# Kernel tuning notes

Measured on AMD Instinct MI355X. Metric: run time of the kernel, lower is better.

## Reference

```python
import jax, jax.numpy as jnp
import numpy as np

B, Q, K, D = 64, 2048, 2048, 128
NEG = -1e9


def setup_inputs() -> dict:
    key = jax.random.key(0)
    kq, kk, kv, kl = jax.random.split(key, 4)
    return {
        "queries": jax.random.normal(kq, (B, Q, D), dtype=jnp.float32),
        "keys": jax.random.normal(kk, (B, K, D), dtype=jnp.float32),
        "values": jax.random.normal(kv, (B, K, D), dtype=jnp.float32),
        "valid_lens": jax.random.randint(kl, (B,), 0, K, dtype=jnp.int32),
    }


def reference(queries, keys, values, valid_lens):
    d = queries.shape[-1]
    # [B, Q, K] scores
    scores = jnp.einsum("bqd,bkd->bqk", queries, keys) / jnp.sqrt(jnp.float32(d))
    # padding mask: position >= valid_len  (mask_softmax valid_lens path)
    positions = jnp.arange(scores.shape[-1], dtype=valid_lens.dtype)
    pad_mask = positions[None, None, :] >= valid_lens[:, None, None]  # [B,1,K] -> bcast over Q
    scores = jnp.where(pad_mask, jnp.float32(NEG), scores)
    attn = jax.nn.softmax(scores, axis=-1)
    out = jnp.einsum("bqk,bkd->bqd", attn, values)  # dropout p=0.0 -> identity
    return (out, attn)
```

## Files before the change

kernel.cpp:

```cpp
#include <hip/hip_runtime.h>
#include <hip/hip_bf16.h>

#define B_N   64
#define Q_N   2048
#define K_N   2048
#define D_N   128
#define NEGV  (-1e9f)
#define SCALE 0.08838834764831845f

using f32x4  = __attribute__((ext_vector_type(4))) float;
using bf16x8 = __attribute__((ext_vector_type(8))) short;

static __device__ __forceinline__ short tobf(float f) {
  __hip_bfloat16 h = __float2bfloat16(f);
  return __builtin_bit_cast(short, h);
}

__global__ __launch_bounds__(256, 2)
void attn_fused(const float* __restrict__ Qg, const float* __restrict__ Kg,
                const float* __restrict__ Vg, const int* __restrict__ vlg,
                float* __restrict__ outp, float* __restrict__ attnp)
{
  __shared__ __align__(16) short Kst[64 * 136];
  __shared__ __align__(16) short Vst[64 * 136];
  __shared__ __align__(16) short Pt [64 * 68];

  const int id   = blockIdx.x;
  const int xcd  = id & 7;
  const int rest = id >> 3;
  const int b    = (rest >> 5) * 8 + xcd;
  const int q0   = (rest & 31) * 64;

  const int tid  = threadIdx.x;
  const int w    = tid >> 6;
  const int lane = tid & 63;
  const int m16  = lane & 15;
  const int quad = lane >> 4;

  const int vlen = vlg[b];
  const int kT   = (vlen == 0) ? K_N : ((vlen + 63) & ~63);

  const float* Qb = Qg + (size_t)b * Q_N * D_N;
  const float* Kb = Kg + (size_t)b * K_N * D_N;
  const float* Vb = Vg + (size_t)b * K_N * D_N;

  {
    float* arow = attnp + ((size_t)b * Q_N + q0 + (tid >> 2)) * K_N;
    const f32x4 z = {0.f, 0.f, 0.f, 0.f};
    for (int col = kT + (tid & 3) * 4; col < K_N; col += 16)
      __builtin_nontemporal_store(z, (f32x4*)(arow + col));
  }

  bf16x8 aQ[4];
  {
    const float* qr = Qb + (size_t)(q0 + w*16 + m16) * D_N + quad*8;
    #pragma unroll
    for (int d0 = 0; d0 < 4; ++d0) {
      float4 f0 = *(const float4*)(qr + d0*32);
      float4 f1 = *(const float4*)(qr + d0*32 + 4);
      bf16x8 a;
      a[0]=tobf(f0.x); a[1]=tobf(f0.y); a[2]=tobf(f0.z); a[3]=tobf(f0.w);
      a[4]=tobf(f1.x); a[5]=tobf(f1.y); a[6]=tobf(f1.z); a[7]=tobf(f1.w);
      aQ[d0] = a;
    }
  }

  auto stage64x128 = [&](const float* __restrict__ srcB, int k0, short* dst) {
    #pragma unroll
    for (int i = 0; i < 4; ++i) {
      int c   = i*256 + tid;
      int row = c >> 4;
      int col = (c & 15) << 3;
      const float* src = srcB + (size_t)(k0 + row) * D_N + col;
      float4 f0 = *(const float4*)(src);
      float4 f1 = *(const float4*)(src + 4);
      bf16x8 v;
      v[0]=tobf(f0.x); v[1]=tobf(f0.y); v[2]=tobf(f0.z); v[3]=tobf(f0.w);
      v[4]=tobf(f1.x); v[5]=tobf(f1.y); v[6]=tobf(f1.z); v[7]=tobf(f1.w);
      *(bf16x8*)&dst[row*136 + col] = v;
    }
  };

  #define QMAX(v) { v = fmaxf(v, __shfl_xor(v, 1)); v = fmaxf(v, __shfl_xor(v, 2)); \
                    v = fmaxf(v, __shfl_xor(v, 4)); v = fmaxf(v, __shfl_xor(v, 8)); }
  #define QSUM(v) { v += __shfl_xor(v, 1); v += __shfl_xor(v, 2); \
                    v += __shfl_xor(v, 4); v += __shfl_xor(v, 8); }

  float m_r[4], l_r[4];
  #pragma unroll
  for (int r = 0; r < 4; ++r) { m_r[r] = -INFINITY; l_r[r] = 0.0f; }

  for (int k0 = 0; k0 < kT; k0 += 64) {
    __syncthreads();
    stage64x128(Kb, k0, Kst);
    __syncthreads();

    f32x4 acc[4];
    #pragma unroll
    for (int kt = 0; kt < 4; ++kt) acc[kt] = (f32x4){0.f,0.f,0.f,0.f};
    #pragma unroll
    for (int kt = 0; kt < 4; ++kt)
      #pragma unroll
      for (int d0 = 0; d0 < 4; ++d0) {
        bf16x8 bk = *(const bf16x8*)&Kst[(kt*16 + m16)*136 + d0*32 + quad*8];
        acc[kt] = __builtin_amdgcn_mfma_f32_16x16x32_bf16(aQ[d0], bk, acc[kt], 0, 0, 0);
      }

    const int key0 = k0 + m16;
    const bool mk0 = (key0     ) >= vlen;
    const bool mk1 = (key0 + 16) >= vlen;
    const bool mk2 = (key0 + 32) >= vlen;
    const bool mk3 = (key0 + 48) >= vlen;
    #pragma unroll
    for (int r = 0; r < 4; ++r) {
      float s0 = mk0 ? NEGV : acc[0][r] * SCALE;
      float s1 = mk1 ? NEGV : acc[1][r] * SCALE;
      float s2 = mk2 ? NEGV : acc[2][r] * SCALE;
      float s3 = mk3 ? NEGV : acc[3][r] * SCALE;
      float tm = fmaxf(fmaxf(s0, s1), fmaxf(s2, s3));
      QMAX(tm);
      float mn = fmaxf(m_r[r], tm);
      float p  = __expf(s0 - mn) + __expf(s1 - mn) + __expf(s2 - mn) + __expf(s3 - mn);
      QSUM(p);
      l_r[r] = l_r[r] * __expf(m_r[r] - mn) + p;
      m_r[r] = mn;
    }
  }
  float inv_l[4];
  #pragma unroll
  for (int r = 0; r < 4; ++r) inv_l[r] = 1.0f / l_r[r];

  f32x4 accO[4][2];
  #pragma unroll
  for (int mt = 0; mt < 4; ++mt)
    #pragma unroll
    for (int nt = 0; nt < 2; ++nt)
      accO[mt][nt] = (f32x4){0.f, 0.f, 0.f, 0.f};

  for (int k0 = 0; k0 < kT; k0 += 64) {
    __syncthreads();
    stage64x128(Kb, k0, Kst);
    stage64x128(Vb, k0, Vst);
    __syncthreads();

    f32x4 acc[4];
    #pragma unroll
    for (int kt = 0; kt < 4; ++kt) acc[kt] = (f32x4){0.f,0.f,0.f,0.f};
    #pragma unroll
    for (int kt = 0; kt < 4; ++kt)
      #pragma unroll
      for (int d0 = 0; d0 < 4; ++d0) {
        bf16x8 bk = *(const bf16x8*)&Kst[(kt*16 + m16)*136 + d0*32 + quad*8];
        acc[kt] = __builtin_amdgcn_mfma_f32_16x16x32_bf16(aQ[d0], bk, acc[kt], 0, 0, 0);
      }

    #pragma unroll
    for (int kt = 0; kt < 4; ++kt) {
      const int key = k0 + kt*16 + m16;
      const bool msk = key >= vlen;
      float pv[4];
      #pragma unroll
      for (int r = 0; r < 4; ++r) {
        float s = msk ? NEGV : acc[kt][r] * SCALE;
        pv[r] = __expf(s - m_r[r]) * inv_l[r];
      }
      float* ap = attnp + ((size_t)b * Q_N + q0 + w*16 + quad*4) * K_N + key;
      #pragma unroll
      for (int r = 0; r < 4; ++r)
        __builtin_nontemporal_store(pv[r], ap + (size_t)r * K_N);
      short4 pk = make_short4(tobf(pv[0]), tobf(pv[1]), tobf(pv[2]), tobf(pv[3]));
      *(short4*)&Pt[(kt*16 + m16)*68 + w*16 + quad*4] = pk;
    }
    __syncthreads();

    #pragma unroll
    for (int c = 0; c < 2; ++c) {
      bf16x8 aP[4];
      #pragma unroll
      for (int mt = 0; mt < 4; ++mt) {
        bf16x8 a;
        #pragma unroll
        for (int j = 0; j < 8; ++j)
          a[j] = Pt[(c*32 + quad*8 + j)*68 + mt*16 + m16];
        aP[mt] = a;
      }
      #pragma unroll
      for (int nt = 0; nt < 2; ++nt) {
        const int vcol = w*32 + nt*16 + m16;
        bf16x8 bv;
        #pragma unroll
        for (int j = 0; j < 8; ++j) bv[j] = Vst[(c*32 + quad*8 + j)*136 + vcol];
        #pragma unroll
        for (int mt = 0; mt < 4; ++mt)
          accO[mt][nt] = __builtin_amdgcn_mfma_f32_16x16x32_bf16(aP[mt], bv, accO[mt][nt], 0, 0, 0);
      }
    }
  }

  #pragma unroll
  for (int mt = 0; mt < 4; ++mt)
    #pragma unroll
    for (int nt = 0; nt < 2; ++nt)
      #pragma unroll
      for (int r = 0; r < 4; ++r) {
        int row = q0 + mt*16 + quad*4 + r;
        int col = w*32 + nt*16 + m16;
        __builtin_nontemporal_store(accO[mt][nt][r],
                                    outp + ((size_t)b * Q_N + row) * D_N + col);
      }
}

extern "C" void kernel_launch(void* const* d_in, const int* in_sizes, int n_in,
                              void* d_out, int out_size, void* d_ws, size_t ws_size,
                              hipStream_t stream) {
  const float* Q  = (const float*)d_in[0];
  const float* K  = (const float*)d_in[1];
  const float* V  = (const float*)d_in[2];
  const int*   vl = (const int*)d_in[3];
  float* outp  = (float*)d_out;
  float* attnp = outp + (size_t)B_N * Q_N * D_N;

  dim3 grid(B_N * (Q_N / 64));
  dim3 block(256);
  hipLaunchKernelGGL(attn_fused, grid, block, 0, stream, Q, K, V, vl, outp, attnp);
}
```

Before: 1.724 ms.

## Prefetch K tiles in registers, drop V LDS staging, swizzle P tile layout

K tiles are now loaded into registers one iteration ahead, so the global loads overlap the score MFMAs. V is no longer staged in shared memory; each lane reads its strided V elements straight from global memory and converts them to bf16. P is stored row-major with an XOR swizzle so the MFMA A operand can be read as one vector load. LDS use drops and occupancy is raised to 4 blocks per CU, at the cost of uncoalesced, duplicated global V reads and more register pressure from the prefetch buffers.

```diff
diff --git a/kernel.cpp b/kernel.cpp
--- a/kernel.cpp
+++ b/kernel.cpp
@@ -16,14 +16,13 @@
   return __builtin_bit_cast(short, h);
 }
 
-__global__ __launch_bounds__(256, 2)
+__global__ __launch_bounds__(256, 4)
 void attn_fused(const float* __restrict__ Qg, const float* __restrict__ Kg,
                 const float* __restrict__ Vg, const int* __restrict__ vlg,
                 float* __restrict__ outp, float* __restrict__ attnp)
 {
   __shared__ __align__(16) short Kst[64 * 136];
-  __shared__ __align__(16) short Vst[64 * 136];
-  __shared__ __align__(16) short Pt [64 * 68];
+  __shared__ __align__(16) short Pst[64 * 72];
 
   const int id   = blockIdx.x;
   const int xcd  = id & 7;
@@ -65,19 +64,24 @@
     }
   }
 
-  auto stage64x128 = [&](const float* __restrict__ srcB, int k0, short* dst) {
+  const int srow = tid >> 4;
+  const int scol = (tid & 15) << 3;
+  float4 kf[4][2];
+  auto load_K = [&](int k0) {
     #pragma unroll
     for (int i = 0; i < 4; ++i) {
-      int c   = i*256 + tid;
-      int row = c >> 4;
-      int col = (c & 15) << 3;
-      const float* src = srcB + (size_t)(k0 + row) * D_N + col;
-      float4 f0 = *(const float4*)(src);
-      float4 f1 = *(const float4*)(src + 4);
+      const float* src = Kb + (size_t)(k0 + i*16 + srow) * D_N + scol;
+      kf[i][0] = *(const float4*)(src);
+      kf[i][1] = *(const float4*)(src + 4);
+    }
+  };
+  auto write_K = [&]() {
+    #pragma unroll
+    for (int i = 0; i < 4; ++i) {
       bf16x8 v;
-      v[0]=tobf(f0.x); v[1]=tobf(f0.y); v[2]=tobf(f0.z); v[3]=tobf(f0.w);
-      v[4]=tobf(f1.x); v[5]=tobf(f1.y); v[6]=tobf(f1.z); v[7]=tobf(f1.w);
-      *(bf16x8*)&dst[row*136 + col] = v;
+      v[0]=tobf(kf[i][0].x); v[1]=tobf(kf[i][0].y); v[2]=tobf(kf[i][0].z); v[3]=tobf(kf[i][0].w);
+      v[4]=tobf(kf[i][1].x); v[5]=tobf(kf[i][1].y); v[6]=tobf(kf[i][1].z); v[7]=tobf(kf[i][1].w);
+      *(bf16x8*)&Kst[(i*16 + srow)*136 + scol] = v;
     }
   };
 
@@ -90,9 +94,11 @@
   #pragma unroll
   for (int r = 0; r < 4; ++r) { m_r[r] = -INFINITY; l_r[r] = 0.0f; }
 
+  load_K(0);
   for (int k0 = 0; k0 < kT; k0 += 64) {
     __syncthreads();
-    stage64x128(Kb, k0, Kst);
+    write_K();
+    if (k0 + 64 < kT) load_K(k0 + 64);
     __syncthreads();
 
     f32x4 acc[4];
@@ -137,10 +143,14 @@
     for (int nt = 0; nt < 2; ++nt)
       accO[mt][nt] = (f32x4){0.f, 0.f, 0.f, 0.f};
 
+  const int pwxor = ((quad >> 1) & 1) << 3;
+  const int prxor = ((m16 >> 3) & 1) << 3;
+
+  load_K(0);
   for (int k0 = 0; k0 < kT; k0 += 64) {
     __syncthreads();
-    stage64x128(Kb, k0, Kst);
-    stage64x128(Vb, k0, Vst);
+    write_K();
+    if (k0 + 64 < kT) load_K(k0 + 64);
     __syncthreads();
 
     f32x4 acc[4];
@@ -168,8 +178,9 @@
       #pragma unroll
       for (int r = 0; r < 4; ++r)
         __builtin_nontemporal_store(pv[r], ap + (size_t)r * K_N);
-      short4 pk = make_short4(tobf(pv[0]), tobf(pv[1]), tobf(pv[2]), tobf(pv[3]));
-      *(short4*)&Pt[(kt*16 + m16)*68 + w*16 + quad*4] = pk;
+      #pragma unroll
+      for (int r = 0; r < 4; ++r)
+        Pst[(((w*16 + quad*4 + r) * 72) + kt*16 + m16) ^ pwxor] = tobf(pv[r]);
     }
     __syncthreads();
 
@@ -177,19 +188,14 @@
     for (int c = 0; c < 2; ++c) {
       bf16x8 aP[4];
       #pragma unroll
-      for (int mt = 0; mt < 4; ++mt) {
-        bf16x8 a;
-        #pragma unroll
-        for (int j = 0; j < 8; ++j)
-          a[j] = Pt[(c*32 + quad*8 + j)*68 + mt*16 + m16];
-        aP[mt] = a;
-      }
+      for (int mt = 0; mt < 4; ++mt)
+        aP[mt] = *(const bf16x8*)&Pst[(((mt*16 + m16) * 72) + c*32 + quad*8) ^ prxor];
       #pragma unroll
       for (int nt = 0; nt < 2; ++nt) {
-        const int vcol = w*32 + nt*16 + m16;
+        const float* vp = Vb + (size_t)(k0 + c*32 + quad*8) * D_N + w*32 + nt*16 + m16;
         bf16x8 bv;
         #pragma unroll
-        for (int j = 0; j < 8; ++j) bv[j] = Vst[(c*32 + quad*8 + j)*136 + vcol];
+        for (int j = 0; j < 8; ++j) bv[j] = tobf(vp[(size_t)j * D_N]);
         #pragma unroll
         for (int mt = 0; mt < 4; ++mt)
           accO[mt][nt] = __builtin_amdgcn_mfma_f32_16x16x32_bf16(aP[mt], bv, accO[mt][nt], 0, 0, 0);
```

After: 1.679 ms. 2.7% less time.
